# Kernel tuning notes

Measured on AMD Instinct MI355X. Metric: run time of the kernel, lower is better.

## Reference

```python
import jax, jax.numpy as jnp
import numpy as np

B, T, H, CH = 8192, 10, 512, 512  # batch, time_step, hidden_size, code_hidden_size (must be equal)


def setup_inputs() -> dict:
    key = jax.random.key(0)
    ks = jax.random.split(key, 18)
    s = 0.05
    inp = {
        "h": jax.random.normal(ks[0], (B, T, CH), dtype=jnp.float32),
        "y_seq": jax.random.normal(ks[1], (B, T), dtype=jnp.float32),
        "attn1_w": jax.random.normal(ks[2], (CH, 2 * H), dtype=jnp.float32) * s,
        "attn1_b": jax.random.normal(ks[3], (CH,), dtype=jnp.float32) * s,
        "attn2_w": jax.random.normal(ks[4], (CH, CH), dtype=jnp.float32) * s,
        "attn2_b": jax.random.normal(ks[5], (CH,), dtype=jnp.float32) * s,
        "attn3_w": jax.random.normal(ks[6], (1, CH), dtype=jnp.float32) * s,
        "attn3_b": jax.random.normal(ks[7], (1,), dtype=jnp.float32) * s,
        "W_ih": jax.random.normal(ks[8], (4 * H, 1), dtype=jnp.float32) * s,
        "W_hh": jax.random.normal(ks[9], (4 * H, H), dtype=jnp.float32) * s,
        "b_ih": jax.random.normal(ks[10], (4 * H,), dtype=jnp.float32) * s,
        "b_hh": jax.random.normal(ks[11], (4 * H,), dtype=jnp.float32) * s,
        "fc1_w": jax.random.normal(ks[12], (H, CH + H), dtype=jnp.float32) * s,
        "fc1_b": jax.random.normal(ks[13], (H,), dtype=jnp.float32) * s,
        "fc2_w": jax.random.normal(ks[14], (1, H), dtype=jnp.float32) * s,
        "fc2_b": jax.random.normal(ks[15], (1,), dtype=jnp.float32) * s,
    }
    return inp


def reference(h, y_seq, attn1_w, attn1_b, attn2_w, attn2_b, attn3_w, attn3_b,
              W_ih, W_hh, b_ih, b_hh, fc1_w, fc1_b, fc2_w, fc2_b):
    # h: [B, T, CH] -> scan over time; y_seq: [B, T]
    h_t = jnp.transpose(h, (1, 0, 2))      # [T, B, CH]
    y_t = jnp.transpose(y_seq, (1, 0))     # [T, B]
    b = h.shape[0]
    hid = W_hh.shape[1]
    d0 = jnp.zeros((b, hid), dtype=h.dtype)
    s0 = jnp.zeros((b, hid), dtype=h.dtype)

    def step(carry, xs):
        d, s = carry
        ht, yt = xs  # ht: [B, CH], yt: [B]
        # attention scores (note: original softmax is over a singleton dim -> weights == 1)
        x = jnp.concatenate([d, ht], axis=1)                       # [B, 2H]
        a = jnp.tanh((x @ attn1_w.T + attn1_b) @ attn2_w.T + attn2_b)
        w = a @ attn3_w.T + attn3_b                                # [B, 1]
        w = jax.nn.softmax(w, axis=1)                              # softmax over size-1 dim == 1
        h1 = w * ht                                                # [B, H] (CH == H)
        # single LSTM step with h0 = h1, c0 = s, input = yt (scalar feature)
        gates = yt[:, None] @ W_ih.T + b_ih + h1 @ W_hh.T + b_hh   # [B, 4H]
        i, f, g, o = jnp.split(gates, 4, axis=1)
        c = jax.nn.sigmoid(f) * s + jax.nn.sigmoid(i) * jnp.tanh(g)
        d_new = jax.nn.sigmoid(o) * jnp.tanh(c)
        return (d_new, c), None

    (d, s), _ = jax.lax.scan(step, (d0, s0), (h_t, y_t))
    z = jnp.concatenate([d, h_t[-1]], axis=1)                      # [B, CH+H]
    y_res = (z @ fc1_w.T + fc1_b) @ fc2_w.T + fc2_b                # [B, 1]
    return y_res
```

## Files before the change

kernel.cpp:

```cpp
#include <hip/hip_runtime.h>
#include <stdint.h>

typedef __attribute__((ext_vector_type(8))) short short8;
typedef __attribute__((ext_vector_type(4))) float f32x4;
typedef unsigned short ushort_t;

#define T_STEPS 10
#define BT 128
#define WPACK_BYTES (2048*1024)
#define VBUF_OFF  WPACK_BYTES
#define HBF_OFF   (WPACK_BYTES + 8192)
#define H_ELEMS   (8192ull*T_STEPS*512)
#define HBF_BYTES (H_ELEMS*2)

typedef const __attribute__((address_space(1))) void gas_void;
typedef __attribute__((address_space(3))) void las_void;

__device__ __forceinline__ void gld_lds16(const void* g, void* l){
  __builtin_amdgcn_global_load_lds((gas_void*)g, (las_void*)l, 16, 0, 0);
}

__device__ __forceinline__ unsigned int pk2(float x, float y){
  unsigned int bx = __float_as_uint(x), by = __float_as_uint(y);
  bx = (bx + 0x7FFFu + ((bx>>16)&1u)) >> 16;
  by = (by + 0x7FFFu + ((by>>16)&1u)) >> 16;
  return bx | (by<<16);
}
__device__ __forceinline__ float sigf(float x){ return 1.f/(1.f + __expf(-x)); }
__device__ __forceinline__ float tanh_(float x){
  x = fminf(fmaxf(x, -15.f), 15.f);
  float e = __expf(2.f*x);
  return (e - 1.f)/(e + 1.f);
}

__global__ __launch_bounds__(256) void k_pack(const float* __restrict__ Whh,
                                              ushort_t* __restrict__ wp){
  int id  = blockIdx.x*256 + threadIdx.x;
  int row = id >> 6;
  int ko  = (id & 63) * 8;
  const float* p = Whh + row*512 + ko;
  float4 a = *(const float4*)p, b = *(const float4*)(p+4);
  uint4 v;
  v.x = pk2(a.x,a.y); v.y = pk2(a.z,a.w);
  v.z = pk2(b.x,b.y); v.w = pk2(b.z,b.w);
  int g = row >> 9, j = row & 511;
  int jb = j >> 6, jt = (j >> 4) & 3, jl = j & 15;
  int kc = ko >> 5, khi = (ko >> 3) & 3, lane = khi*16 + jl;
  int chunk = ((jb*4 + jt)*4 + g)*16 + kc;
  *(uint4*)(wp + chunk*512 + lane*8) = v;
}

__global__ __launch_bounds__(256) void k_v(const float* __restrict__ fc1w,
                                           const float* __restrict__ fc1b,
                                           const float* __restrict__ fc2w,
                                           const float* __restrict__ fc2b,
                                           float* __restrict__ vout,
                                           float* __restrict__ bias0){
  __shared__ float red[4][64];
  int tid = threadIdx.x;
  if (blockIdx.x < 16){
    int j  = blockIdx.x*64 + (tid & 63);
    int hc = tid >> 6;
    float s = 0.f;
    for (int hh = hc*128; hh < hc*128 + 128; ++hh)
      s += fc2w[hh] * fc1w[hh*1024 + j];
    red[hc][tid & 63] = s;
    __syncthreads();
    if (tid < 64)
      vout[blockIdx.x*64 + tid] = red[0][tid]+red[1][tid]+red[2][tid]+red[3][tid];
  } else {
    if (tid < 64){
      float s = 0.f;
      for (int i = 0; i < 8; ++i){ int hh = i*64 + tid; s += fc2w[hh]*fc1b[hh]; }
      for (int m = 32; m; m >>= 1) s += __shfl_xor(s, m);
      if (tid == 0) *bias0 = s + fc2b[0];
    }
  }
}

__global__ __launch_bounds__(512) void k_init(const float* __restrict__ h,
                                              const float* __restrict__ v,
                                              const float* __restrict__ bias0,
                                              float* __restrict__ out){
  int w = threadIdx.x >> 6, lane = threadIdx.x & 63;
  float b0v = *bias0;
  const float* v2 = v + 512;
  for (int r = 0; r < 8; ++r){
    int b = blockIdx.x*64 + w*8 + r;
    const float* hp = h + ((size_t)b*T_STEPS + 9)*512 + lane*8;
    float4 x0 = *(const float4*)hp, x1 = *(const float4*)(hp+4);
    const float* vp = v2 + lane*8;
    float4 w0 = *(const float4*)vp, w1 = *(const float4*)(vp+4);
    float s = x0.x*w0.x + x0.y*w0.y + x0.z*w0.z + x0.w*w0.w
            + x1.x*w1.x + x1.y*w1.y + x1.z*w1.z + x1.w*w1.w;
    for (int m = 32; m; m >>= 1) s += __shfl_xor(s, m);
    if (lane == 0) out[b] = s + b0v;
  }
}

__global__ __launch_bounds__(256) void k_prep(const float* __restrict__ h,
                                              ushort_t* __restrict__ hbf){
  __shared__ __align__(16) ushort_t buf[16*512*8];
  int T = blockIdx.x / T_STEPS, t = blockIdx.x % T_STEPS;
  int tid = threadIdx.x;
  int row = tid >> 1, half = tid & 1;
  const float* src = h + ((size_t)(T*128 + row)*T_STEPS + t)*512 + half*256;
#pragma unroll
  for (int g = 0; g < 32; ++g){
    int k0 = half*256 + g*8;
    float4 a = *(const float4*)(src + g*8);
    float4 b = *(const float4*)(src + g*8 + 4);
    uint4 pk;
    pk.x = pk2(a.x,a.y); pk.y = pk2(a.z,a.w);
    pk.z = pk2(b.x,b.y); pk.w = pk2(b.z,b.w);
    int kc = k0 >> 5, kq = (k0 >> 3) & 3;
    *(uint4*)&buf[(size_t)(kc*512 + kq*128 + row)*8] = pk;
  }
  __syncthreads();
  ushort_t* dst = hbf + ((size_t)(T*T_STEPS + t)*16)*4096;
#pragma unroll
  for (int i = 0; i < 32; ++i){
    int gr = tid + i*256;
    *(uint4*)(dst + gr*8) = *(const uint4*)&buf[gr*8];
  }
}

template<bool PREP>
__global__ __launch_bounds__(256)
__attribute__((amdgpu_waves_per_eu(2, 2)))
void k_main(
    const float* __restrict__ h, const ushort_t* __restrict__ hbf,
    const float* __restrict__ y,
    const float* __restrict__ Wih, const float* __restrict__ bih,
    const float* __restrict__ bhh,
    const ushort_t* __restrict__ wpack, const float* __restrict__ v1,
    float* __restrict__ out)
{
  __shared__ __align__(16) ushort_t Ab[2][4096];
  __shared__ float ys[BT*T_STEPS];

  int tid = threadIdx.x;
  int w = tid >> 6, lane = tid & 63, lhi = lane >> 4, llo = lane & 15;
  int mh = w & 1, wj = w >> 1;
  int bid = blockIdx.x;
  int xcd = bid & 7, q = bid >> 3;
  int jb = q >> 3, tile = xcd*8 + (q & 7);
  int b0 = tile * BT;

  float bias2[4][2], wihv[4][2], v1v[2];
#pragma unroll
  for (int g = 0; g < 4; ++g)
#pragma unroll
    for (int n = 0; n < 2; ++n){
      int col = g*512 + jb*64 + (wj*2+n)*16 + llo;
      bias2[g][n] = bih[col] + bhh[col];
      wihv[g][n]  = Wih[col];
    }
#pragma unroll
  for (int n = 0; n < 2; ++n) v1v[n] = v1[jb*64 + (wj*2+n)*16 + llo];

  for (int i = tid; i < BT*T_STEPS; i += 256)
    ys[i] = y[(size_t)b0*T_STEPS + i];

  const ushort_t* asrc = hbf + (size_t)tile*(T_STEPS*16)*4096 + (w*128 + lane)*8;
  const ushort_t* wbase = wpack + (size_t)(jb*4 + wj*2)*4*8192 + lane*8;

  auto stageA = [&](int parity){
    if constexpr (PREP){
      gld_lds16(asrc,       &Ab[parity][w*1024]);
      gld_lds16(asrc + 512, &Ab[parity][w*1024 + 512]);
      asrc += 4096;
    }
  };
  auto stageA_f = [&](int parity, int ss){
    int t = (ss < 160) ? (ss >> 4) : 9;
    int kc = ss & 15;
#pragma unroll
    for (int i = 0; i < 2; ++i){
      int gidx = tid + i*256;
      int kq = gidx >> 7, row = gidx & 127;
      const float* p = h + ((size_t)(b0+row)*T_STEPS + t)*512 + kc*32 + kq*8;
      float4 x0 = *(const float4*)p, x1 = *(const float4*)(p+4);
      uint4 pk;
      pk.x = pk2(x0.x,x0.y); pk.y = pk2(x0.z,x0.w);
      pk.z = pk2(x1.x,x1.y); pk.w = pk2(x1.z,x1.w);
      *(uint4*)&Ab[parity][gidx*8] = pk;
    }
  };

  if constexpr (PREP) stageA(0); else stageA_f(0, 0);
  __syncthreads();

  f32x4 acc[4][3][2];
  float cst[4][2][4];
#pragma unroll
  for (int m = 0; m < 4; ++m)
#pragma unroll
    for (int n = 0; n < 2; ++n){
#pragma unroll
      for (int g = 0; g < 3; ++g) acc[m][g][n] = (f32x4){0.f,0.f,0.f,0.f};
#pragma unroll
      for (int r = 0; r < 4; ++r) cst[m][n][r] = 0.f;
    }

  const int aro = (lhi*128 + mh*64 + llo)*8;

#pragma unroll 1
  for (int s = 0; s < 160; ++s){
    if (s < 159){
      if constexpr (PREP) stageA((s+1)&1); else stageA_f((s+1)&1, s+1);
    } else {
      if constexpr (PREP) { asrc -= 16*4096; stageA(0); }
      else stageA_f(0, 160);
    }

    int kco = (s & 15) * 512;
    short8 wf[3][2];
#pragma unroll
    for (int g = 0; g < 3; ++g)
#pragma unroll
      for (int n = 0; n < 2; ++n)
        wf[g][n] = *(const short8*)(wbase + (size_t)(n*4+g)*8192 + kco);

    const ushort_t* ap = &Ab[s&1][aro];
    short8 af[4];
#pragma unroll
    for (int m = 0; m < 4; ++m)
      af[m] = *(const short8*)(ap + m*128);

#pragma unroll
    for (int g = 0; g < 3; ++g)
#pragma unroll
      for (int n = 0; n < 2; ++n)
#pragma unroll
        for (int m = 0; m < 4; ++m)
          acc[m][g][n] = __builtin_amdgcn_mfma_f32_16x16x32_bf16(
              af[m], wf[g][n], acc[m][g][n], 0, 0, 0);

    if ((s & 15) == 15){
      int t = s >> 4;
#pragma unroll
      for (int m = 0; m < 4; ++m)
#pragma unroll
        for (int r = 0; r < 4; ++r){
          float yr = ys[(mh*64 + m*16 + lhi*4 + r)*T_STEPS + t];
#pragma unroll
          for (int n = 0; n < 2; ++n){
            float pi = acc[m][0][n][r] + fmaf(yr, wihv[0][n], bias2[0][n]);
            float pf = acc[m][1][n][r] + fmaf(yr, wihv[1][n], bias2[1][n]);
            float pg = acc[m][2][n][r] + fmaf(yr, wihv[2][n], bias2[2][n]);
            cst[m][n][r] = sigf(pf)*cst[m][n][r] + sigf(pi)*tanh_(pg);
          }
        }
#pragma unroll
      for (int m = 0; m < 4; ++m)
#pragma unroll
        for (int g = 0; g < 3; ++g)
#pragma unroll
          for (int n = 0; n < 2; ++n) acc[m][g][n] = (f32x4){0.f,0.f,0.f,0.f};
    }
    __syncthreads();
  }

  f32x4 acco[4][2];
#pragma unroll
  for (int m = 0; m < 4; ++m)
#pragma unroll
    for (int n = 0; n < 2; ++n) acco[m][n] = (f32x4){0.f,0.f,0.f,0.f};

#pragma unroll 1
  for (int s2 = 0; s2 < 16; ++s2){
    if (s2 < 15){
      if constexpr (PREP) stageA((s2+1)&1); else stageA_f((s2+1)&1, 161+s2);
    }
    int kco = s2 * 512;
    short8 wo[2];
#pragma unroll
    for (int n = 0; n < 2; ++n)
      wo[n] = *(const short8*)(wbase + (size_t)(n*4+3)*8192 + kco);

    const ushort_t* ap = &Ab[s2&1][aro];
    short8 af[4];
#pragma unroll
    for (int m = 0; m < 4; ++m)
      af[m] = *(const short8*)(ap + m*128);
#pragma unroll
    for (int n = 0; n < 2; ++n)
#pragma unroll
      for (int m = 0; m < 4; ++m)
        acco[m][n] = __builtin_amdgcn_mfma_f32_16x16x32_bf16(
            af[m], wo[n], acco[m][n], 0, 0, 0);
    __syncthreads();
  }

#pragma unroll
  for (int m = 0; m < 4; ++m)
#pragma unroll
    for (int r = 0; r < 4; ++r){
      float yr = ys[(mh*64 + m*16 + lhi*4 + r)*T_STEPS + 9];
      float val = 0.f;
#pragma unroll
      for (int n = 0; n < 2; ++n){
        float po = acco[m][n][r] + fmaf(yr, wihv[3][n], bias2[3][n]);
        val += sigf(po)*tanh_(cst[m][n][r])*v1v[n];
      }
      val += __shfl_xor(val, 1);
      val += __shfl_xor(val, 2);
      val += __shfl_xor(val, 4);
      val += __shfl_xor(val, 8);
      if (llo == 0)
        atomicAdd(&out[b0 + mh*64 + m*16 + lhi*4 + r], val);
    }
}

extern "C" void kernel_launch(void* const* d_in, const int* in_sizes, int n_in,
                              void* d_out, int out_size, void* d_ws, size_t ws_size,
                              hipStream_t stream){
  (void)in_sizes; (void)n_in; (void)out_size;
  const float* h    = (const float*)d_in[0];
  const float* y    = (const float*)d_in[1];
  const float* Wih  = (const float*)d_in[8];
  const float* Whh  = (const float*)d_in[9];
  const float* bih  = (const float*)d_in[10];
  const float* bhh  = (const float*)d_in[11];
  const float* fc1w = (const float*)d_in[12];
  const float* fc1b = (const float*)d_in[13];
  const float* fc2w = (const float*)d_in[14];
  const float* fc2b = (const float*)d_in[15];
  float* out = (float*)d_out;

  ushort_t* wpack = (ushort_t*)d_ws;
  float* vbuf  = (float*)((char*)d_ws + VBUF_OFF);
  float* bias0 = vbuf + 1024;
  ushort_t* hbf = (ushort_t*)((char*)d_ws + HBF_OFF);
  bool prep = ws_size >= (size_t)HBF_OFF + HBF_BYTES;

  k_pack<<<512, 256, 0, stream>>>(Whh, wpack);
  k_v<<<17, 256, 0, stream>>>(fc1w, fc1b, fc2w, fc2b, vbuf, bias0);
  if (prep)
    k_prep<<<64*T_STEPS, 256, 0, stream>>>(h, hbf);
  k_init<<<128, 512, 0, stream>>>(h, vbuf, bias0, out);
  if (prep)
    k_main<true ><<<512, 256, 0, stream>>>(h, hbf, y, Wih, bih, bhh, wpack, vbuf, out);
  else
    k_main<false><<<512, 256, 0, stream>>>(h, hbf, y, Wih, bih, bhh, wpack, vbuf, out);
}
```

Baseline: 276.1 us.

## Load A fragments directly from global into registers, dropping LDS staging and barriers

The prepped-path main kernel no longer stages bf16 h tiles through double-buffered LDS with per-step barriers. Each wave now loads its A and W fragments straight from global memory into registers, using a two-deep software prefetch (A/B register sets) across the K loop. This removes LDS traffic and __syncthreads from the inner loop. In exchange it adds register pressure and duplicate global loads of A across waves that share rows, which rely on the cache.

```diff
diff --git a/kernel.cpp b/kernel.cpp
--- a/kernel.cpp
+++ b/kernel.cpp
@@ -125,18 +125,14 @@
   }
 }
 
-template<bool PREP>
 __global__ __launch_bounds__(256)
 __attribute__((amdgpu_waves_per_eu(2, 2)))
-void k_main(
-    const float* __restrict__ h, const ushort_t* __restrict__ hbf,
-    const float* __restrict__ y,
-    const float* __restrict__ Wih, const float* __restrict__ bih,
-    const float* __restrict__ bhh,
-    const ushort_t* __restrict__ wpack, const float* __restrict__ v1,
-    float* __restrict__ out)
+void k_main_r(const ushort_t* __restrict__ hbf, const float* __restrict__ y,
+              const float* __restrict__ Wih, const float* __restrict__ bih,
+              const float* __restrict__ bhh,
+              const ushort_t* __restrict__ wpack, const float* __restrict__ v1,
+              float* __restrict__ out)
 {
-  __shared__ __align__(16) ushort_t Ab[2][4096];
   __shared__ float ys[BT*T_STEPS];
 
   int tid = threadIdx.x;
@@ -161,17 +157,202 @@
 
   for (int i = tid; i < BT*T_STEPS; i += 256)
     ys[i] = y[(size_t)b0*T_STEPS + i];
-
-  const ushort_t* asrc = hbf + (size_t)tile*(T_STEPS*16)*4096 + (w*128 + lane)*8;
-  const ushort_t* wbase = wpack + (size_t)(jb*4 + wj*2)*4*8192 + lane*8;
-
-  auto stageA = [&](int parity){
-    if constexpr (PREP){
-      gld_lds16(asrc,       &Ab[parity][w*1024]);
-      gld_lds16(asrc + 512, &Ab[parity][w*1024 + 512]);
-      asrc += 4096;
-    }
-  };
+  __syncthreads();
+
+  const ushort_t* abase = hbf + (size_t)tile*655360
+                        + (size_t)(lhi*128 + mh*64 + llo)*8;
+  const ushort_t* wbase = wpack + (size_t)(jb*4 + wj*2)*32768 + lane*8;
+
+  f32x4 acc[4][3][2];
+  float cst[4][2][4];
+#pragma unroll
+  for (int m = 0; m < 4; ++m)
+#pragma unroll
+    for (int n = 0; n < 2; ++n){
+#pragma unroll
+      for (int g = 0; g < 3; ++g) acc[m][g][n] = (f32x4){0.f,0.f,0.f,0.f};
+#pragma unroll
+      for (int r = 0; r < 4; ++r) cst[m][n][r] = 0.f;
+    }
+
+  const ushort_t* aT = abase;
+#pragma unroll 1
+  for (int t = 0; t < T_STEPS; ++t){
+    short8 afA[4], wfA[3][2], afB[4], wfB[3][2];
+    const ushort_t* ap = aT;
+    const ushort_t* wk = wbase;
+
+#pragma unroll
+    for (int m = 0; m < 4; ++m) afA[m] = *(const short8*)(ap + m*128);
+#pragma unroll
+    for (int g = 0; g < 3; ++g)
+#pragma unroll
+      for (int n = 0; n < 2; ++n)
+        wfA[g][n] = *(const short8*)(wk + (size_t)(n*4+g)*8192);
+
+#pragma unroll 1
+    for (int kp = 0; kp < 8; ++kp){
+#pragma unroll
+      for (int m = 0; m < 4; ++m) afB[m] = *(const short8*)(ap + 4096 + m*128);
+#pragma unroll
+      for (int g = 0; g < 3; ++g)
+#pragma unroll
+        for (int n = 0; n < 2; ++n)
+          wfB[g][n] = *(const short8*)(wk + (size_t)(n*4+g)*8192 + 512);
+#pragma unroll
+      for (int g = 0; g < 3; ++g)
+#pragma unroll
+        for (int n = 0; n < 2; ++n)
+#pragma unroll
+          for (int m = 0; m < 4; ++m)
+            acc[m][g][n] = __builtin_amdgcn_mfma_f32_16x16x32_bf16(
+                afA[m], wfA[g][n], acc[m][g][n], 0, 0, 0);
+      if (kp < 7){
+#pragma unroll
+        for (int m = 0; m < 4; ++m) afA[m] = *(const short8*)(ap + 8192 + m*128);
+#pragma unroll
+        for (int g = 0; g < 3; ++g)
+#pragma unroll
+          for (int n = 0; n < 2; ++n)
+            wfA[g][n] = *(const short8*)(wk + (size_t)(n*4+g)*8192 + 1024);
+      }
+#pragma unroll
+      for (int g = 0; g < 3; ++g)
+#pragma unroll
+        for (int n = 0; n < 2; ++n)
+#pragma unroll
+          for (int m = 0; m < 4; ++m)
+            acc[m][g][n] = __builtin_amdgcn_mfma_f32_16x16x32_bf16(
+                afB[m], wfB[g][n], acc[m][g][n], 0, 0, 0);
+      ap += 8192;
+      wk += 1024;
+    }
+
+#pragma unroll
+    for (int m = 0; m < 4; ++m)
+#pragma unroll
+      for (int r = 0; r < 4; ++r){
+        float yr = ys[(mh*64 + m*16 + lhi*4 + r)*T_STEPS + t];
+#pragma unroll
+        for (int n = 0; n < 2; ++n){
+          float pi = acc[m][0][n][r] + fmaf(yr, wihv[0][n], bias2[0][n]);
+          float pf = acc[m][1][n][r] + fmaf(yr, wihv[1][n], bias2[1][n]);
+          float pg = acc[m][2][n][r] + fmaf(yr, wihv[2][n], bias2[2][n]);
+          cst[m][n][r] = sigf(pf)*cst[m][n][r] + sigf(pi)*tanh_(pg);
+        }
+      }
+#pragma unroll
+    for (int m = 0; m < 4; ++m)
+#pragma unroll
+      for (int g = 0; g < 3; ++g)
+#pragma unroll
+        for (int n = 0; n < 2; ++n) acc[m][g][n] = (f32x4){0.f,0.f,0.f,0.f};
+
+    aT += 65536;
+  }
+
+  f32x4 acco[4][2];
+#pragma unroll
+  for (int m = 0; m < 4; ++m)
+#pragma unroll
+    for (int n = 0; n < 2; ++n) acco[m][n] = (f32x4){0.f,0.f,0.f,0.f};
+
+  {
+    const ushort_t* ap = abase + (size_t)9*65536;
+    const ushort_t* wk = wbase + (size_t)3*8192;
+    short8 afA[4], woA[2], afB[4], woB[2];
+#pragma unroll
+    for (int m = 0; m < 4; ++m) afA[m] = *(const short8*)(ap + m*128);
+#pragma unroll
+    for (int n = 0; n < 2; ++n) woA[n] = *(const short8*)(wk + (size_t)n*32768);
+
+#pragma unroll 1
+    for (int kp = 0; kp < 8; ++kp){
+#pragma unroll
+      for (int m = 0; m < 4; ++m) afB[m] = *(const short8*)(ap + 4096 + m*128);
+#pragma unroll
+      for (int n = 0; n < 2; ++n)
+        woB[n] = *(const short8*)(wk + (size_t)n*32768 + 512);
+#pragma unroll
+      for (int n = 0; n < 2; ++n)
+#pragma unroll
+        for (int m = 0; m < 4; ++m)
+          acco[m][n] = __builtin_amdgcn_mfma_f32_16x16x32_bf16(
+              afA[m], woA[n], acco[m][n], 0, 0, 0);
+      if (kp < 7){
+#pragma unroll
+        for (int m = 0; m < 4; ++m) afA[m] = *(const short8*)(ap + 8192 + m*128);
+#pragma unroll
+        for (int n = 0; n < 2; ++n)
+          woA[n] = *(const short8*)(wk + (size_t)n*32768 + 1024);
+      }
+#pragma unroll
+      for (int n = 0; n < 2; ++n)
+#pragma unroll
+        for (int m = 0; m < 4; ++m)
+          acco[m][n] = __builtin_amdgcn_mfma_f32_16x16x32_bf16(
+              afB[m], woB[n], acco[m][n], 0, 0, 0);
+      ap += 8192;
+      wk += 1024;
+    }
+  }
+
+#pragma unroll
+  for (int m = 0; m < 4; ++m)
+#pragma unroll
+    for (int r = 0; r < 4; ++r){
+      float yr = ys[(mh*64 + m*16 + lhi*4 + r)*T_STEPS + 9];
+      float val = 0.f;
+#pragma unroll
+      for (int n = 0; n < 2; ++n){
+        float po = acco[m][n][r] + fmaf(yr, wihv[3][n], bias2[3][n]);
+        val += sigf(po)*tanh_(cst[m][n][r])*v1v[n];
+      }
+      val += __shfl_xor(val, 1);
+      val += __shfl_xor(val, 2);
+      val += __shfl_xor(val, 4);
+      val += __shfl_xor(val, 8);
+      if (llo == 0)
+        atomicAdd(&out[b0 + mh*64 + m*16 + lhi*4 + r], val);
+    }
+}
+
+__global__ __launch_bounds__(256)
+__attribute__((amdgpu_waves_per_eu(2, 2)))
+void k_main_f(const float* __restrict__ h, const float* __restrict__ y,
+              const float* __restrict__ Wih, const float* __restrict__ bih,
+              const float* __restrict__ bhh,
+              const ushort_t* __restrict__ wpack, const float* __restrict__ v1,
+              float* __restrict__ out)
+{
+  __shared__ __align__(16) ushort_t Ab[2][4096];
+  __shared__ float ys[BT*T_STEPS];
+
+  int tid = threadIdx.x;
+  int w = tid >> 6, lane = tid & 63, lhi = lane >> 4, llo = lane & 15;
+  int mh = w & 1, wj = w >> 1;
+  int bid = blockIdx.x;
+  int xcd = bid & 7, q = bid >> 3;
+  int jb = q >> 3, tile = xcd*8 + (q & 7);
+  int b0 = tile * BT;
+
+  float bias2[4][2], wihv[4][2], v1v[2];
+#pragma unroll
+  for (int g = 0; g < 4; ++g)
+#pragma unroll
+    for (int n = 0; n < 2; ++n){
+      int col = g*512 + jb*64 + (wj*2+n)*16 + llo;
+      bias2[g][n] = bih[col] + bhh[col];
+      wihv[g][n]  = Wih[col];
+    }
+#pragma unroll
+  for (int n = 0; n < 2; ++n) v1v[n] = v1[jb*64 + (wj*2+n)*16 + llo];
+
+  for (int i = tid; i < BT*T_STEPS; i += 256)
+    ys[i] = y[(size_t)b0*T_STEPS + i];
+
+  const ushort_t* wbase = wpack + (size_t)(jb*4 + wj*2)*32768 + lane*8;
+
   auto stageA_f = [&](int parity, int ss){
     int t = (ss < 160) ? (ss >> 4) : 9;
     int kc = ss & 15;
@@ -188,7 +369,7 @@
     }
   };
 
-  if constexpr (PREP) stageA(0); else stageA_f(0, 0);
+  stageA_f(0, 0);
   __syncthreads();
 
   f32x4 acc[4][3][2];
@@ -207,12 +388,8 @@
 
 #pragma unroll 1
   for (int s = 0; s < 160; ++s){
-    if (s < 159){
-      if constexpr (PREP) stageA((s+1)&1); else stageA_f((s+1)&1, s+1);
-    } else {
-      if constexpr (PREP) { asrc -= 16*4096; stageA(0); }
-      else stageA_f(0, 160);
-    }
+    if (s < 159) stageA_f((s+1)&1, s+1);
+    else         stageA_f(0, 160);
 
     int kco = (s & 15) * 512;
     short8 wf[3][2];
@@ -270,9 +447,7 @@
 
 #pragma unroll 1
   for (int s2 = 0; s2 < 16; ++s2){
-    if (s2 < 15){
-      if constexpr (PREP) stageA((s2+1)&1); else stageA_f((s2+1)&1, 161+s2);
-    }
+    if (s2 < 15) stageA_f((s2+1)&1, 161+s2);
     int kco = s2 * 512;
     short8 wo[2];
 #pragma unroll
@@ -341,7 +516,7 @@
     k_prep<<<64*T_STEPS, 256, 0, stream>>>(h, hbf);
   k_init<<<128, 512, 0, stream>>>(h, vbuf, bias0, out);
   if (prep)
-    k_main<true ><<<512, 256, 0, stream>>>(h, hbf, y, Wih, bih, bhh, wpack, vbuf, out);
+    k_main_r<<<512, 256, 0, stream>>>(hbf, y, Wih, bih, bhh, wpack, vbuf, out);
   else
-    k_main<false><<<512, 256, 0, stream>>>(h, hbf, y, Wih, bih, bhh, wpack, vbuf, out);
-}
+    k_main_f<<<512, 256, 0, stream>>>(h, y, Wih, bih, bhh, wpack, vbuf, out);
+}
```

New measurement: 254.0 us. -8.0%, faster.
